# Kernel optimization log

Hardware: AMD Instinct MI355X
Metric: run time of the kernel (lower is better)

## Reference

```python
import jax, jax.numpy as jnp
import numpy as np

B, S, D, H = 2, 2048, 1024, 16
DH = D // H  # 64


def setup_inputs() -> dict:
    key = jax.random.key(0)
    ks = jax.random.split(key, 9)
    scale = 0.02
    x = jax.random.normal(ks[0], (B, S, D), dtype=jnp.float32)
    # per-head QKV weights stacked over heads: [H, D, DH]
    Wq = jax.random.normal(ks[1], (H, D, DH), dtype=jnp.float32) * scale
    Wk = jax.random.normal(ks[2], (H, D, DH), dtype=jnp.float32) * scale
    Wv = jax.random.normal(ks[3], (H, D, DH), dtype=jnp.float32) * scale
    bq = jax.random.normal(ks[4], (H, DH), dtype=jnp.float32) * scale
    bk = jax.random.normal(ks[5], (H, DH), dtype=jnp.float32) * scale
    bv = jax.random.normal(ks[6], (H, DH), dtype=jnp.float32) * scale
    Wo = jax.random.normal(ks[7], (D, D), dtype=jnp.float32) * scale
    bo = jax.random.normal(ks[8], (D,), dtype=jnp.float32) * scale
    return {"x": x, "Wq": Wq, "bq": bq, "Wk": Wk, "bk": bk, "Wv": Wv, "bv": bv, "Wo": Wo, "bo": bo}


def reference(x, Wq, bq, Wk, bk, Wv, bv, Wo, bo):
    # per-head projections: [B, H, S, DH]
    q = jnp.einsum('bsd,hde->bhse', x, Wq) + bq[None, :, None, :]
    k = jnp.einsum('bsd,hde->bhse', x, Wk) + bk[None, :, None, :]
    v = jnp.einsum('bsd,hde->bhse', x, Wv) + bv[None, :, None, :]
    scores = jnp.einsum('bhse,bhte->bhst', q, k) / jnp.sqrt(jnp.float32(DH))
    probs = jax.nn.softmax(scores, axis=-1)  # [B, H, S, S]
    ctx = jnp.einsum('bhst,bhte->bhse', probs, v)  # [B, H, S, DH]
    # concat heads: [B, S, H*DH]
    ctx = jnp.transpose(ctx, (0, 2, 1, 3)).reshape(x.shape[0], x.shape[1], H * DH)
    out = ctx @ Wo + bo  # output projection; dropout p=0 -> identity
    return out
```

## Files before the change

kernel.cpp:

```cpp
#include <hip/hip_runtime.h>

typedef __attribute__((ext_vector_type(8))) short short8;
typedef __attribute__((ext_vector_type(4))) float f32x4;
typedef __attribute__((ext_vector_type(16))) float f32x16;
typedef __attribute__((ext_vector_type(4))) unsigned short us4;
typedef unsigned short ushort;

typedef __attribute__((address_space(3))) void lds_void;
typedef __attribute__((address_space(1))) void gbl_void;

__device__ __forceinline__ ushort f2bf(float f) {
  unsigned u = __float_as_uint(f);
  u += 0x7fff + ((u >> 16) & 1);
  return (ushort)(u >> 16);
}

__global__ void cvt_x_kernel(const float* __restrict__ x, ushort* __restrict__ xb) {
  int i = (blockIdx.x * 256 + threadIdx.x) * 8;
  float4 a = *(const float4*)(x + i);
  float4 b = *(const float4*)(x + i + 4);
  ushort o[8];
  o[0] = f2bf(a.x); o[1] = f2bf(a.y); o[2] = f2bf(a.z); o[3] = f2bf(a.w);
  o[4] = f2bf(b.x); o[5] = f2bf(b.y); o[6] = f2bf(b.z); o[7] = f2bf(b.w);
  *(short8*)(xb + i) = *(short8*)o;
}

__global__ void wprep_kernel(const float* __restrict__ Wq, const float* __restrict__ Wk,
                             const float* __restrict__ Wv, const float* __restrict__ Wo,
                             ushort* __restrict__ wqkv_t, ushort* __restrict__ wo_t) {
  __shared__ float T[64][65];
  const int k0 = blockIdx.x * 64;
  const int hy = blockIdx.y;
  const int m = blockIdx.z;
  const float* src = (m == 0) ? Wq : (m == 1) ? Wk : (m == 2) ? Wv : Wo;
#pragma unroll
  for (int it = 0; it < 16; ++it) {
    int idx = it * 256 + threadIdx.x;
    int kk = idx >> 6, e = idx & 63;
    float v = (m < 3) ? src[hy * 65536 + (k0 + kk) * 64 + e]
                      : src[(k0 + kk) * 1024 + hy * 64 + e];
    T[e][kk] = v;
  }
  __syncthreads();
  ushort* dst = (m < 3) ? (wqkv_t + (size_t)(m * 1024 + hy * 64) * 1024)
                        : (wo_t + (size_t)(hy * 64) * 1024);
#pragma unroll
  for (int it = 0; it < 2; ++it) {
    int c = it * 256 + threadIdx.x;
    int e = c >> 3, kc = (c & 7) * 8;
    ushort o[8];
#pragma unroll
    for (int j = 0; j < 8; ++j) o[j] = f2bf(T[e][kc + j]);
    *(short8*)&dst[(size_t)e * 1024 + k0 + kc] = *(short8*)o;
  }
}

__global__ __launch_bounds__(512, 2) void gemm_qkv256(
    const ushort* __restrict__ A, const ushort* __restrict__ Bt,
    const float* __restrict__ b0, const float* __restrict__ b1, const float* __restrict__ b2,
    ushort* __restrict__ qfp, ushort* __restrict__ kfp, ushort* __restrict__ vfp) {
  __shared__ ushort sm[3][2][256][32];
  const int tid = threadIdx.x;
  const int lane = tid & 63;
  const int wave = tid >> 6;
  const int l15 = lane & 15, l4 = lane >> 4;
  const int wwr = wave >> 2, wc = wave & 3;
  const int p0 = blockIdx.x;
  const int p = (p0 & 7) * 24 + (p0 >> 3);
  const int by = p & 15, bx = p >> 4;
  const int row0 = by * 256, col0 = bx * 256;

  const ushort* Ag = A + (size_t)row0 * 1024;
  const ushort* Bg = Bt + (size_t)col0 * 1024;
  char* smb = (char*)&sm[0][0][0][0];

  auto stage = [&](int buf, int kt, int c0) {
    const int c = c0 + tid;
    const int row = (c & 1023) >> 2;
    const int slot = c & 3;
    const int scol = (slot ^ ((row >> 1) & 3)) * 8;
    const ushort* src = ((c >> 10) ? Bg : Ag) + (size_t)row * 1024 + kt * 32 + scol;
    __builtin_amdgcn_global_load_lds((const gbl_void*)src,
        (lds_void*)(smb + buf * 32768 + (c0 + (tid & ~63)) * 16), 16, 0, 0);
  };
  auto rdA = [&](int buf, int mfg) {
    const int row = wwr * 128 + mfg * 16 + l15;
    return *(const short8*)(smb + buf * 32768 + row * 64 + ((l4 ^ ((row >> 1) & 3)) << 4));
  };
  auto rdB = [&](int buf, int nf) {
    const int row = wc * 64 + nf * 16 + l15;
    return *(const short8*)(smb + buf * 32768 + 16384 + row * 64 + ((l4 ^ ((row >> 1) & 3)) << 4));
  };

  f32x4 acc[8][4];
#pragma unroll
  for (int i = 0; i < 8; ++i)
#pragma unroll
    for (int j = 0; j < 4; ++j) acc[i][j] = (f32x4){0.f, 0.f, 0.f, 0.f};

  stage(0, 0, 0); stage(0, 0, 512); stage(0, 0, 1024); stage(0, 0, 1536);
  stage(1, 1, 0); stage(1, 1, 512); stage(1, 1, 1024); stage(1, 1, 1536);

  int buf = 0;
  for (int kt = 0; kt < 32; ++kt) {
    if (kt == 31) asm volatile("s_waitcnt vmcnt(0)" ::: "memory");
    else          asm volatile("s_waitcnt vmcnt(4)" ::: "memory");
    asm volatile("s_barrier" ::: "memory");
    const int kn = kt + 2;
    const int bn = (buf >= 1) ? buf - 1 : buf + 2;
    short8 bfr[4], af[4];
#pragma unroll
    for (int nf = 0; nf < 4; ++nf) bfr[nf] = rdB(buf, nf);
#pragma unroll
    for (int mf = 0; mf < 4; ++mf) af[mf] = rdA(buf, mf);
    if (kn < 32) { stage(bn, kn, 0); stage(bn, kn, 512); }
    __builtin_amdgcn_s_setprio(1);
#pragma unroll
    for (int mf = 0; mf < 4; ++mf)
#pragma unroll
      for (int nf = 0; nf < 4; ++nf)
        acc[mf][nf] = __builtin_amdgcn_mfma_f32_16x16x32_bf16(af[mf], bfr[nf], acc[mf][nf], 0, 0, 0);
    __builtin_amdgcn_s_setprio(0);
    asm volatile("s_barrier" ::: "memory");
#pragma unroll
    for (int mf = 0; mf < 4; ++mf) af[mf] = rdA(buf, 4 + mf);
    if (kn < 32) { stage(bn, kn, 1024); stage(bn, kn, 1536); }
    __builtin_amdgcn_s_setprio(1);
#pragma unroll
    for (int mf = 0; mf < 4; ++mf)
#pragma unroll
      for (int nf = 0; nf < 4; ++nf)
        acc[4 + mf][nf] = __builtin_amdgcn_mfma_f32_16x16x32_bf16(af[mf], bfr[nf], acc[4 + mf][nf], 0, 0, 0);
    __builtin_amdgcn_s_setprio(0);
    buf = (buf == 2) ? 0 : buf + 1;
  }

  const float QSCALE = 0.18033688f;
#pragma unroll
  for (int mfg = 0; mfg < 8; ++mfg) {
    const int row = row0 + wwr * 128 + mfg * 16 + l4 * 4;
    const int bb = row >> 11, s = row & 2047;
#pragma unroll
    for (int nf = 0; nf < 4; ++nf) {
      const int col = col0 + wc * 64 + nf * 16 + l15;
      if (col < 2048) {
        const int cf = col & 1023;
        const int h = cf >> 6, d = cf & 63;
        const int bh = bb * 16 + h;
        ushort* dst = (col < 1024) ? qfp : kfp;
        const float bias = ((col < 1024) ? b0 : b1)[cf];
        const float sc = (col < 1024) ? QSCALE : 1.0f;
        const size_t base =
            ((((size_t)bh * 64 + (s >> 5)) * 4 + (d >> 4)) * 64 + ((d >> 3) & 1) * 32 + (s & 31)) * 8 +
            (d & 7);
#pragma unroll
        for (int r = 0; r < 4; ++r) dst[base + r * 8] = f2bf((acc[mfg][nf][r] + bias) * sc);
      } else {
        const int ef = col - 2048;
        const int h = ef >> 6, e = ef & 63;
        const int bh = bb * 16 + h;
        const float bias = b2[ef];
        ushort o4[4];
#pragma unroll
        for (int r = 0; r < 4; ++r) o4[r] = f2bf(acc[mfg][nf][r] + bias);
        const size_t addr =
            ((((size_t)bh * 2 + (e >> 5)) * 128 + (s >> 4)) * 64 + ((s >> 3) & 1) * 32 + (e & 31)) * 8 +
            (s & 7);
        *(us4*)&vfp[addr] = *(us4*)o4;
      }
    }
  }
}

__global__ __launch_bounds__(256) void gemm_out_kernel(
    const ushort* __restrict__ A, const ushort* __restrict__ Bt,
    const float* __restrict__ b0, float* __restrict__ C) {
  __shared__ ushort lA[128 * 32];
  __shared__ ushort lB[128 * 32];
  const int tid = threadIdx.x;
  const int lane = tid & 63;
  const int wave = tid >> 6;
  const int l15 = lane & 15, l4 = lane >> 4;
  const int wr = wave >> 1, wc = wave & 1;
  const int row0 = blockIdx.y * 128, col0 = blockIdx.x * 128;

  f32x4 acc[4][4];
#pragma unroll
  for (int i = 0; i < 4; ++i)
#pragma unroll
    for (int j = 0; j < 4; ++j) acc[i][j] = (f32x4){0.f, 0.f, 0.f, 0.f};

  const ushort* Ag = A + (size_t)row0 * 1024;
  const ushort* Bg = Bt + (size_t)col0 * 1024;

  for (int k0 = 0; k0 < 1024; k0 += 32) {
#pragma unroll
    for (int c = 0; c < 2; ++c) {
      const int chunk = tid + c * 256;
      const int rr = chunk >> 2;
      const int kc = (chunk & 3) * 8;
      const unsigned lbase = (unsigned)((tid & ~63) + c * 256) * 16;
      __builtin_amdgcn_global_load_lds((const gbl_void*)(Ag + (size_t)rr * 1024 + k0 + kc),
                                       (lds_void*)((char*)lA + lbase), 16, 0, 0);
      __builtin_amdgcn_global_load_lds((const gbl_void*)(Bg + (size_t)rr * 1024 + k0 + kc),
                                       (lds_void*)((char*)lB + lbase), 16, 0, 0);
    }
    __syncthreads();
    short8 af[4], bfr[4];
#pragma unroll
    for (int i = 0; i < 4; ++i)
      af[i] = *(const short8*)&lA[(wr * 64 + i * 16 + l15) * 32 + l4 * 8];
#pragma unroll
    for (int j = 0; j < 4; ++j)
      bfr[j] = *(const short8*)&lB[(wc * 64 + j * 16 + l15) * 32 + l4 * 8];
#pragma unroll
    for (int i = 0; i < 4; ++i)
#pragma unroll
      for (int j = 0; j < 4; ++j)
        acc[i][j] = __builtin_amdgcn_mfma_f32_16x16x32_bf16(af[i], bfr[j], acc[i][j], 0, 0, 0);
    __syncthreads();
  }

#pragma unroll
  for (int i = 0; i < 4; ++i) {
    const int row = row0 + wr * 64 + i * 16 + l4 * 4;
#pragma unroll
    for (int j = 0; j < 4; ++j) {
      const int col = col0 + wc * 64 + j * 16 + l15;
      const float bias = b0[col];
#pragma unroll
      for (int r = 0; r < 4; ++r)
        C[(size_t)(row + r) * 1024 + col] = acc[i][j][r] + bias;
    }
  }
}

__global__ __launch_bounds__(512, 2) void attn_kernel(const ushort* __restrict__ qf,
                                                      const ushort* __restrict__ kf,
                                                      const ushort* __restrict__ vf,
                                                      ushort* __restrict__ ctx) {
  __shared__ ushort sm[2][2][8192];
  const int tid = threadIdx.x;
  const int lane = tid & 63, wave = tid >> 6;
  const int grp = wave >> 2, gw = wave & 3;
  const int gtid = tid & 255;
  const int l31 = lane & 31, hi = lane >> 5;
  const int p0 = blockIdx.x;
  const int idx = p0 >> 3;
  const int bh = (p0 & 7) * 4 + (idx >> 4);
  const int q0 = ((idx & 15) * 4 + gw) * 32;
  const int b = bh >> 4, h = bh & 15;

  const size_t bhbase = (size_t)bh * 131072;
  const ushort* qfb = qf + bhbase + (size_t)(q0 >> 5) * 2048 + (size_t)lane * 8;
  const ushort* kfbh = kf + bhbase;
  const ushort* vfbh = vf + bhbase;
  char* gsm = (char*)&sm[grp][0][0];

  short8 qb[4];
#pragma unroll
  for (int kk = 0; kk < 4; ++kk)
    qb[kk] = *(const short8*)(qfb + kk * 512);

  auto stage = [&](int buf, int t0) {
    const ushort* s0 = kfbh + (size_t)(t0 >> 5) * 2048 + gtid * 8;
    const ushort* s1 = s0 + 2048;
    const ushort* s2 = vfbh + (size_t)(t0 >> 4) * 512 + gtid * 8;
    const ushort* s3 = s2 + 65536;
    char* d = gsm + buf * 16384 + (gtid & ~63) * 16;
    __builtin_amdgcn_global_load_lds((const gbl_void*)s0, (lds_void*)(d), 16, 0, 0);
    __builtin_amdgcn_global_load_lds((const gbl_void*)s1, (lds_void*)(d + 4096), 16, 0, 0);
    __builtin_amdgcn_global_load_lds((const gbl_void*)s2, (lds_void*)(d + 8192), 16, 0, 0);
    __builtin_amdgcn_global_load_lds((const gbl_void*)s3, (lds_void*)(d + 12288), 16, 0, 0);
  };

  f32x16 cacc[2];
#pragma unroll
  for (int me = 0; me < 2; ++me)
#pragma unroll
    for (int r = 0; r < 16; ++r) cacc[me][r] = 0.f;
  float l_run = 0.f;

  const int tbase = grp * 1024;
  stage(0, tbase);
  for (int it = 0; it < 16; ++it) {
    asm volatile("s_waitcnt vmcnt(0)" ::: "memory");
    asm volatile("s_barrier" ::: "memory");
    if (it < 15) stage((it + 1) & 1, tbase + (it + 1) * 64);

    const char* kb = gsm + (it & 1) * 16384;
    const char* vb = kb + 8192;

    short8 ka[2][4];
#pragma unroll
    for (int me = 0; me < 2; ++me)
#pragma unroll
      for (int kk = 0; kk < 4; ++kk)
        ka[me][kk] = *(const short8*)(kb + me * 4096 + kk * 1024 + lane * 16);

    f32x16 sacc[2];
    __builtin_amdgcn_s_setprio(1);
#pragma unroll
    for (int me = 0; me < 2; ++me) {
#pragma unroll
      for (int r = 0; r < 16; ++r) sacc[me][r] = 0.f;
#pragma unroll
      for (int kk = 0; kk < 4; ++kk)
        sacc[me] = __builtin_amdgcn_mfma_f32_32x32x16_bf16(ka[me][kk], qb[kk], sacc[me], 0, 0, 0);
    }
    __builtin_amdgcn_s_setprio(0);

    float s0 = 0.f, s1 = 0.f, s2 = 0.f, s3 = 0.f;
    unsigned w[2][8];
#pragma unroll
    for (int me = 0; me < 2; ++me) {
      float pp[16];
#pragma unroll
      for (int r = 0; r < 16; r += 4) {
        pp[r + 0] = __builtin_amdgcn_exp2f(sacc[me][r + 0]);
        pp[r + 1] = __builtin_amdgcn_exp2f(sacc[me][r + 1]);
        pp[r + 2] = __builtin_amdgcn_exp2f(sacc[me][r + 2]);
        pp[r + 3] = __builtin_amdgcn_exp2f(sacc[me][r + 3]);
        s0 += pp[r + 0]; s1 += pp[r + 1]; s2 += pp[r + 2]; s3 += pp[r + 3];
      }
#pragma unroll
      for (int i = 0; i < 8; ++i)
        asm("v_cvt_pk_bf16_f32 %0, %1, %2" : "=v"(w[me][i]) : "v"(pp[2 * i]), "v"(pp[2 * i + 1]));
    }
    l_run += (s0 + s1) + (s2 + s3);

    unsigned pb[4][4];
#pragma unroll
    for (int me = 0; me < 2; ++me)
#pragma unroll
      for (int c = 0; c < 2; ++c) {
        unsigned a0 = w[me][4 * c + 0], a1 = w[me][4 * c + 1];
        unsigned b0r = w[me][4 * c + 2], b1r = w[me][4 * c + 3];
        asm("v_permlane32_swap_b32 %0, %1" : "+v"(a0), "+v"(b0r));
        asm("v_permlane32_swap_b32 %0, %1" : "+v"(a1), "+v"(b1r));
        const int kk = me * 2 + c;
        pb[kk][0] = a0; pb[kk][1] = a1; pb[kk][2] = b0r; pb[kk][3] = b1r;
      }

    short8 va[2][4];
#pragma unroll
    for (int mev = 0; mev < 2; ++mev)
#pragma unroll
      for (int kk = 0; kk < 4; ++kk)
        va[mev][kk] = *(const short8*)(vb + mev * 4096 + kk * 1024 + lane * 16);

    __builtin_amdgcn_s_setprio(1);
#pragma unroll
    for (int mev = 0; mev < 2; ++mev)
#pragma unroll
      for (int kk = 0; kk < 4; ++kk)
        cacc[mev] = __builtin_amdgcn_mfma_f32_32x32x16_bf16(va[mev][kk], *(const short8*)&pb[kk][0],
                                                            cacc[mev], 0, 0, 0);
    __builtin_amdgcn_s_setprio(0);
  }

  l_run += __shfl_xor(l_run, 32);
  __syncthreads();
  float* mb = (float*)&sm[0][0][0];
  if (grp == 1) {
#pragma unroll
    for (int mev = 0; mev < 2; ++mev)
#pragma unroll
      for (int r = 0; r < 16; ++r)
        mb[(mev * 16 + r) * 256 + gw * 64 + lane] = cacc[mev][r];
    mb[8192 + gw * 64 + lane] = l_run;
  }
  __syncthreads();
  if (grp == 0) {
    const float l1 = mb[8192 + gw * 64 + lane];
    const float inv = 1.f / (l_run + l1);
    const int q = q0 + l31;
#pragma unroll
    for (int mev = 0; mev < 2; ++mev)
#pragma unroll
      for (int g = 0; g < 4; ++g) {
        ushort o4[4];
#pragma unroll
        for (int rr = 0; rr < 4; ++rr) {
          const int r = g * 4 + rr;
          const float v = (cacc[mev][r] + mb[(mev * 16 + r) * 256 + gw * 64 + lane]) * inv;
          o4[rr] = f2bf(v);
        }
        const int e0 = mev * 32 + 8 * g + 4 * hi;
        *(us4*)&ctx[(size_t)(b * 2048 + q) * 1024 + h * 64 + e0] = *(us4*)o4;
      }
  }
}

extern "C" void kernel_launch(void* const* d_in, const int* in_sizes, int n_in,
                              void* d_out, int out_size, void* d_ws, size_t ws_size,
                              hipStream_t stream) {
  const float* x = (const float*)d_in[0];
  const float* Wq = (const float*)d_in[1];
  const float* bq = (const float*)d_in[2];
  const float* Wk = (const float*)d_in[3];
  const float* bk = (const float*)d_in[4];
  const float* Wv = (const float*)d_in[5];
  const float* bv = (const float*)d_in[6];
  const float* Wo = (const float*)d_in[7];
  const float* bo = (const float*)d_in[8];
  float* out = (float*)d_out;

  char* ws = (char*)d_ws;
  ushort* xb = (ushort*)ws;
  ushort* ctx = xb;
  ushort* wqkv_t = (ushort*)(ws + 8u * 1024 * 1024);
  ushort* wo_t = (ushort*)(ws + 14u * 1024 * 1024);
  ushort* qf = (ushort*)(ws + 16u * 1024 * 1024);
  ushort* kf = (ushort*)(ws + 24u * 1024 * 1024);
  ushort* vf = (ushort*)(ws + 32u * 1024 * 1024);

  cvt_x_kernel<<<dim3(2048), dim3(256), 0, stream>>>(x, xb);
  wprep_kernel<<<dim3(16, 16, 4), dim3(256), 0, stream>>>(Wq, Wk, Wv, Wo, wqkv_t, wo_t);
  gemm_qkv256<<<dim3(192), dim3(512), 0, stream>>>(xb, wqkv_t, bq, bk, bv, qf, kf, vf);
  attn_kernel<<<dim3(512), dim3(512), 0, stream>>>(qf, kf, vf, ctx);
  gemm_out_kernel<<<dim3(8, 32), dim3(256), 0, stream>>>(ctx, wo_t, bo, out);
}
```

Measured before the change: 117.9 us.

## Triple-buffer output GEMM with swizzled LDS and packed softmax sums in attention

The output-projection GEMM moves from a single LDS buffer with two barriers per k-step to a three-stage ring. Two tiles are prefetched ahead with partial vmcnt waits, and the LDS layout is XOR-swizzled to reduce bank conflicts on fragment reads. The attention kernel now advances its K/V staging pointers incrementally, seeds the first MFMA from a zero register instead of re-zeroing the accumulator, and accumulates row sums with packed v_pk_add_f32. The GEMM triples its LDS use, which may lower occupancy, and the inline asm adds scheduling constraints.

Measured after the change: 111.9 us. -5.1%, faster.

```diff
diff --git a/kernel.cpp b/kernel.cpp
--- a/kernel.cpp
+++ b/kernel.cpp
@@ -1,6 +1,7 @@
 #include <hip/hip_runtime.h>
 
 typedef __attribute__((ext_vector_type(8))) short short8;
+typedef __attribute__((ext_vector_type(2))) float f32x2;
 typedef __attribute__((ext_vector_type(4))) float f32x4;
 typedef __attribute__((ext_vector_type(16))) float f32x16;
 typedef __attribute__((ext_vector_type(4))) unsigned short us4;
@@ -175,8 +176,7 @@
 __global__ __launch_bounds__(256) void gemm_out_kernel(
     const ushort* __restrict__ A, const ushort* __restrict__ Bt,
     const float* __restrict__ b0, float* __restrict__ C) {
-  __shared__ ushort lA[128 * 32];
-  __shared__ ushort lB[128 * 32];
+  __shared__ ushort sm[3][2][128][32];
   const int tid = threadIdx.x;
   const int lane = tid & 63;
   const int wave = tid >> 6;
@@ -184,41 +184,58 @@
   const int wr = wave >> 1, wc = wave & 1;
   const int row0 = blockIdx.y * 128, col0 = blockIdx.x * 128;
 
-  f32x4 acc[4][4];
-#pragma unroll
-  for (int i = 0; i < 4; ++i)
-#pragma unroll
-    for (int j = 0; j < 4; ++j) acc[i][j] = (f32x4){0.f, 0.f, 0.f, 0.f};
-
   const ushort* Ag = A + (size_t)row0 * 1024;
   const ushort* Bg = Bt + (size_t)col0 * 1024;
-
-  for (int k0 = 0; k0 < 1024; k0 += 32) {
-#pragma unroll
-    for (int c = 0; c < 2; ++c) {
-      const int chunk = tid + c * 256;
-      const int rr = chunk >> 2;
-      const int kc = (chunk & 3) * 8;
-      const unsigned lbase = (unsigned)((tid & ~63) + c * 256) * 16;
-      __builtin_amdgcn_global_load_lds((const gbl_void*)(Ag + (size_t)rr * 1024 + k0 + kc),
-                                       (lds_void*)((char*)lA + lbase), 16, 0, 0);
-      __builtin_amdgcn_global_load_lds((const gbl_void*)(Bg + (size_t)rr * 1024 + k0 + kc),
-                                       (lds_void*)((char*)lB + lbase), 16, 0, 0);
-    }
-    __syncthreads();
+  char* smb = (char*)&sm[0][0][0][0];
+
+  auto stage = [&](int buf, int kt, int c0) {
+    const int c = c0 + tid;
+    const int row = (c & 511) >> 2;
+    const int slot = c & 3;
+    const int scol = (slot ^ ((row >> 1) & 3)) * 8;
+    const ushort* src = ((c >> 9) ? Bg : Ag) + (size_t)row * 1024 + kt * 32 + scol;
+    __builtin_amdgcn_global_load_lds((const gbl_void*)src,
+        (lds_void*)(smb + buf * 16384 + (c0 + (tid & ~63)) * 16), 16, 0, 0);
+  };
+  auto rdA = [&](int buf, int mf) {
+    const int row = wr * 64 + mf * 16 + l15;
+    return *(const short8*)(smb + buf * 16384 + row * 64 + ((l4 ^ ((row >> 1) & 3)) << 4));
+  };
+  auto rdB = [&](int buf, int nf) {
+    const int row = wc * 64 + nf * 16 + l15;
+    return *(const short8*)(smb + buf * 16384 + 8192 + row * 64 + ((l4 ^ ((row >> 1) & 3)) << 4));
+  };
+
+  f32x4 acc[4][4];
+#pragma unroll
+  for (int i = 0; i < 4; ++i)
+#pragma unroll
+    for (int j = 0; j < 4; ++j) acc[i][j] = (f32x4){0.f, 0.f, 0.f, 0.f};
+
+  stage(0, 0, 0); stage(0, 0, 256); stage(0, 0, 512); stage(0, 0, 768);
+  stage(1, 1, 0); stage(1, 1, 256); stage(1, 1, 512); stage(1, 1, 768);
+
+  int buf = 0;
+  for (int kt = 0; kt < 32; ++kt) {
+    if (kt == 31) asm volatile("s_waitcnt vmcnt(0)" ::: "memory");
+    else          asm volatile("s_waitcnt vmcnt(4)" ::: "memory");
+    asm volatile("s_barrier" ::: "memory");
+    const int kn = kt + 2;
+    const int bn = (buf >= 1) ? buf - 1 : buf + 2;
     short8 af[4], bfr[4];
 #pragma unroll
-    for (int i = 0; i < 4; ++i)
-      af[i] = *(const short8*)&lA[(wr * 64 + i * 16 + l15) * 32 + l4 * 8];
-#pragma unroll
-    for (int j = 0; j < 4; ++j)
-      bfr[j] = *(const short8*)&lB[(wc * 64 + j * 16 + l15) * 32 + l4 * 8];
-#pragma unroll
-    for (int i = 0; i < 4; ++i)
-#pragma unroll
-      for (int j = 0; j < 4; ++j)
-        acc[i][j] = __builtin_amdgcn_mfma_f32_16x16x32_bf16(af[i], bfr[j], acc[i][j], 0, 0, 0);
-    __syncthreads();
+    for (int nf = 0; nf < 4; ++nf) bfr[nf] = rdB(buf, nf);
+#pragma unroll
+    for (int mf = 0; mf < 4; ++mf) af[mf] = rdA(buf, mf);
+    if (kn < 32) { stage(bn, kn, 0); stage(bn, kn, 256); stage(bn, kn, 512); stage(bn, kn, 768); }
+    __builtin_amdgcn_s_setprio(1);
+#pragma unroll
+    for (int mf = 0; mf < 4; ++mf)
+#pragma unroll
+      for (int nf = 0; nf < 4; ++nf)
+        acc[mf][nf] = __builtin_amdgcn_mfma_f32_16x16x32_bf16(af[mf], bfr[nf], acc[mf][nf], 0, 0, 0);
+    __builtin_amdgcn_s_setprio(0);
+    buf = (buf == 2) ? 0 : buf + 1;
   }
 
 #pragma unroll
@@ -253,25 +270,24 @@
 
   const size_t bhbase = (size_t)bh * 131072;
   const ushort* qfb = qf + bhbase + (size_t)(q0 >> 5) * 2048 + (size_t)lane * 8;
-  const ushort* kfbh = kf + bhbase;
-  const ushort* vfbh = vf + bhbase;
   char* gsm = (char*)&sm[grp][0][0];
+  char* dbase = gsm + (gtid & ~63) * 16;
 
   short8 qb[4];
 #pragma unroll
   for (int kk = 0; kk < 4; ++kk)
     qb[kk] = *(const short8*)(qfb + kk * 512);
 
-  auto stage = [&](int buf, int t0) {
-    const ushort* s0 = kfbh + (size_t)(t0 >> 5) * 2048 + gtid * 8;
-    const ushort* s1 = s0 + 2048;
-    const ushort* s2 = vfbh + (size_t)(t0 >> 4) * 512 + gtid * 8;
-    const ushort* s3 = s2 + 65536;
-    char* d = gsm + buf * 16384 + (gtid & ~63) * 16;
-    __builtin_amdgcn_global_load_lds((const gbl_void*)s0, (lds_void*)(d), 16, 0, 0);
-    __builtin_amdgcn_global_load_lds((const gbl_void*)s1, (lds_void*)(d + 4096), 16, 0, 0);
-    __builtin_amdgcn_global_load_lds((const gbl_void*)s2, (lds_void*)(d + 8192), 16, 0, 0);
-    __builtin_amdgcn_global_load_lds((const gbl_void*)s3, (lds_void*)(d + 12288), 16, 0, 0);
+  const int tbase = grp * 1024;
+  const ushort* kp = kf + bhbase + (size_t)(tbase >> 5) * 2048 + gtid * 8;
+  const ushort* vp = vf + bhbase + (size_t)(tbase >> 4) * 512 + gtid * 8;
+
+  auto stage2 = [&](int buf, const ushort* kpp, const ushort* vpp) {
+    char* d = dbase + buf * 16384;
+    __builtin_amdgcn_global_load_lds((const gbl_void*)kpp, (lds_void*)(d), 16, 0, 0);
+    __builtin_amdgcn_global_load_lds((const gbl_void*)(kpp + 2048), (lds_void*)(d + 4096), 16, 0, 0);
+    __builtin_amdgcn_global_load_lds((const gbl_void*)(vpp), (lds_void*)(d + 8192), 16, 0, 0);
+    __builtin_amdgcn_global_load_lds((const gbl_void*)(vpp + 65536), (lds_void*)(d + 12288), 16, 0, 0);
   };
 
   f32x16 cacc[2];
@@ -279,14 +295,17 @@
   for (int me = 0; me < 2; ++me)
 #pragma unroll
     for (int r = 0; r < 16; ++r) cacc[me][r] = 0.f;
-  float l_run = 0.f;
-
-  const int tbase = grp * 1024;
-  stage(0, tbase);
+  f32x16 fz;
+#pragma unroll
+  for (int r = 0; r < 16; ++r) fz[r] = 0.f;
+  f32x2 l2a = {0.f, 0.f}, l2b = {0.f, 0.f}, l2c = {0.f, 0.f}, l2d = {0.f, 0.f};
+
+  stage2(0, kp, vp);
   for (int it = 0; it < 16; ++it) {
     asm volatile("s_waitcnt vmcnt(0)" ::: "memory");
     asm volatile("s_barrier" ::: "memory");
-    if (it < 15) stage((it + 1) & 1, tbase + (it + 1) * 64);
+    if (it < 15) stage2((it + 1) & 1, kp + 4096, vp + 2048);
+    kp += 4096; vp += 2048;
 
     const char* kb = gsm + (it & 1) * 16384;
     const char* vb = kb + 8192;
@@ -302,32 +321,34 @@
     __builtin_amdgcn_s_setprio(1);
 #pragma unroll
     for (int me = 0; me < 2; ++me) {
-#pragma unroll
-      for (int r = 0; r < 16; ++r) sacc[me][r] = 0.f;
-#pragma unroll
-      for (int kk = 0; kk < 4; ++kk)
+      sacc[me] = __builtin_amdgcn_mfma_f32_32x32x16_bf16(ka[me][0], qb[0], fz, 0, 0, 0);
+#pragma unroll
+      for (int kk = 1; kk < 4; ++kk)
         sacc[me] = __builtin_amdgcn_mfma_f32_32x32x16_bf16(ka[me][kk], qb[kk], sacc[me], 0, 0, 0);
     }
     __builtin_amdgcn_s_setprio(0);
 
-    float s0 = 0.f, s1 = 0.f, s2 = 0.f, s3 = 0.f;
     unsigned w[2][8];
 #pragma unroll
     for (int me = 0; me < 2; ++me) {
-      float pp[16];
-#pragma unroll
-      for (int r = 0; r < 16; r += 4) {
-        pp[r + 0] = __builtin_amdgcn_exp2f(sacc[me][r + 0]);
-        pp[r + 1] = __builtin_amdgcn_exp2f(sacc[me][r + 1]);
-        pp[r + 2] = __builtin_amdgcn_exp2f(sacc[me][r + 2]);
-        pp[r + 3] = __builtin_amdgcn_exp2f(sacc[me][r + 3]);
-        s0 += pp[r + 0]; s1 += pp[r + 1]; s2 += pp[r + 2]; s3 += pp[r + 3];
+      f32x2 pq[8];
+#pragma unroll
+      for (int j = 0; j < 8; ++j) {
+        pq[j][0] = __builtin_amdgcn_exp2f(sacc[me][2 * j]);
+        pq[j][1] = __builtin_amdgcn_exp2f(sacc[me][2 * j + 1]);
       }
-#pragma unroll
-      for (int i = 0; i < 8; ++i)
-        asm("v_cvt_pk_bf16_f32 %0, %1, %2" : "=v"(w[me][i]) : "v"(pp[2 * i]), "v"(pp[2 * i + 1]));
+      asm("v_pk_add_f32 %0, %1, %2" : "=v"(l2a) : "v"(pq[0]), "v"(l2a));
+      asm("v_pk_add_f32 %0, %1, %2" : "=v"(l2b) : "v"(pq[1]), "v"(l2b));
+      asm("v_pk_add_f32 %0, %1, %2" : "=v"(l2c) : "v"(pq[2]), "v"(l2c));
+      asm("v_pk_add_f32 %0, %1, %2" : "=v"(l2d) : "v"(pq[3]), "v"(l2d));
+      asm("v_pk_add_f32 %0, %1, %2" : "=v"(l2a) : "v"(pq[4]), "v"(l2a));
+      asm("v_pk_add_f32 %0, %1, %2" : "=v"(l2b) : "v"(pq[5]), "v"(l2b));
+      asm("v_pk_add_f32 %0, %1, %2" : "=v"(l2c) : "v"(pq[6]), "v"(l2c));
+      asm("v_pk_add_f32 %0, %1, %2" : "=v"(l2d) : "v"(pq[7]), "v"(l2d));
+#pragma unroll
+      for (int j = 0; j < 8; ++j)
+        asm("v_cvt_pk_bf16_f32 %0, %1, %2" : "=v"(w[me][j]) : "v"(pq[j][0]), "v"(pq[j][1]));
     }
-    l_run += (s0 + s1) + (s2 + s3);
 
     unsigned pb[4][4];
 #pragma unroll
@@ -359,6 +380,7 @@
     __builtin_amdgcn_s_setprio(0);
   }
 
+  float l_run = (l2a[0] + l2a[1]) + (l2b[0] + l2b[1]) + (l2c[0] + l2c[1]) + (l2d[0] + l2d[1]);
   l_run += __shfl_xor(l_run, 32);
   __syncthreads();
   float* mb = (float*)&sm[0][0][0];
```
